# Kernel tuning notes

Hardware: AMD Instinct MI355X
Metric: run time of the kernel (lower is better)

The kernel has to match this reference:

```python
import jax, jax.numpy as jnp
import numpy as np

B, S, P, N, V = 8, 16, 32, 2048, 2562
K_SAMPLE = 500      # samples_per_slot
K_NEAREST = 3
MIN_DIST = 0.5
FALLOFF = 5.0
GW, SW, RW = 0.7, 0.3, 0.2


def _icosphere(level=4):
    t = (1.0 + 5.0 ** 0.5) / 2.0
    v = np.array([[-1, t, 0], [1, t, 0], [-1, -t, 0], [1, -t, 0],
                  [0, -1, t], [0, 1, t], [0, -1, -t], [0, 1, -t],
                  [t, 0, -1], [t, 0, 1], [-t, 0, -1], [-t, 0, 1]], dtype=np.float64)
    v /= np.linalg.norm(v, axis=1, keepdims=True)
    f = [[0, 11, 5], [0, 5, 1], [0, 1, 7], [0, 7, 10], [0, 10, 11],
         [1, 5, 9], [5, 11, 4], [11, 10, 2], [10, 7, 6], [7, 1, 8],
         [3, 9, 4], [3, 4, 2], [3, 2, 6], [3, 6, 8], [3, 8, 9],
         [4, 9, 5], [2, 4, 11], [6, 2, 10], [8, 6, 7], [9, 8, 1]]
    verts = [x for x in v]
    for _ in range(level):
        cache = {}
        def mid(a, b):
            key = (min(a, b), max(a, b))
            if key in cache:
                return cache[key]
            m = verts[a] + verts[b]
            m = m / np.linalg.norm(m)
            verts.append(m)
            cache[key] = len(verts) - 1
            return cache[key]
        nf = []
        for a, b, c in f:
            ab, bc, ca = mid(a, b), mid(b, c), mid(c, a)
            nf += [[a, ab, ca], [b, bc, ab], [c, ca, bc], [ab, bc, ca]]
        f = nf
    return np.asarray(verts, dtype=np.float32)


def _euler_xyz_to_matrix(ang):
    # pytorch3d euler_angles_to_matrix(..., 'XYZ'): R = Rx(a) @ Ry(b) @ Rz(c)
    a, b, c = ang[..., 0], ang[..., 1], ang[..., 2]
    ca, sa = jnp.cos(a), jnp.sin(a)
    cb, sb = jnp.cos(b), jnp.sin(b)
    cc, sc = jnp.cos(c), jnp.sin(c)
    o, z = jnp.ones_like(a), jnp.zeros_like(a)
    sh = ang.shape[:-1] + (3, 3)
    Rx = jnp.stack([o, z, z, z, ca, -sa, z, sa, ca], -1).reshape(sh)
    Ry = jnp.stack([cb, z, sb, z, o, z, -sb, z, cb], -1).reshape(sh)
    Rz = jnp.stack([cc, -sc, z, sc, cc, z, z, z, o], -1).reshape(sh)
    return Rx @ Ry @ Rz


def _cdist2(x, y):
    # squared euclidean distances: x [..., n, 3], y [..., m, 3] -> [..., n, m]
    x2 = (x * x).sum(-1)[..., :, None]
    y2 = (y * y).sum(-1)[..., None, :]
    return jnp.maximum(x2 + y2 - 2.0 * jnp.einsum('...nd,...md->...nm', x, y), 0.0)


def _forward(scales, transforms, prototype_weights, prototype_offsets, target_pcl, verts):
    # --- transform_mesh ---
    R = _euler_xyz_to_matrix(transforms[..., 3:])          # [B,S,P,3,3]
    deformed = verts[None] + prototype_offsets              # [P,V,3]
    rotated = jnp.einsum('pvj,bspij->bspvi', deformed, R)   # verts @ R^T
    scaled = rotated * scales[:, :, None, None, :]          # [B,S,P,V,3]
    translated = scaled + transforms[:, :, :, None, :3]
    final = jnp.einsum('bspvi,bsp->bsvi', translated, prototype_weights)  # [B,S,V,3]

    # --- hybrid chamfer loss ---
    pred = final[:, :, :K_SAMPLE, :]                        # deterministic per-slot samples
    pred_flat = pred.reshape(B, S * K_SAMPLE, 3)
    # global: target -> all predicted points, mean of K nearest squared dists
    d2g = _cdist2(target_pcl, pred_flat)                    # [B,N,S*K]
    knn = -jax.lax.top_k(-d2g, K_NEAREST)[0]
    global_loss = knn.mean()
    # per-slot: each slot's points -> target, nearest neighbor squared dist
    d2s = _cdist2(pred, target_pcl[:, None])                # [B,S,K,N]
    per_slot_loss = d2s.min(-1).mean()
    # centroid repulsion
    cent = final.mean(axis=2)                               # [B,S,3]
    eye = jnp.eye(S, dtype=final.dtype)
    d = jnp.sqrt(_cdist2(cent, cent) + eye)                 # eye keeps diag grads finite
    rep = jnp.exp(FALLOFF * jnp.maximum(MIN_DIST - d, 0.0)) * (1.0 - eye)
    rep_loss = (rep.sum(axis=(1, 2)) / (S * (S - 1))).mean()

    return GW * global_loss + SW * per_slot_loss + RW * rep_loss


def setup_inputs() -> dict:
    key = jax.random.key(0)
    ks = jax.random.split(key, 5)
    scales = jax.random.uniform(ks[0], (B, S, 1), jnp.float32) * 0.5 + 0.5
    transforms = jax.random.normal(ks[1], (B, S, P, 6), jnp.float32)
    w = jax.random.uniform(ks[2], (B, S, P), jnp.float32) + 1e-3
    prototype_weights = w / w.sum(-1, keepdims=True)
    prototype_offsets = jax.random.normal(ks[3], (P, V, 3), jnp.float32) * 0.1
    target_pcl = jax.random.normal(ks[4], (B, N, 3), jnp.float32)
    verts = jnp.asarray(_icosphere(4))                      # [2562,3]
    return {"scales": scales, "transforms": transforms,
            "prototype_weights": prototype_weights,
            "prototype_offsets": prototype_offsets,
            "target_pcl": target_pcl, "verts": verts}


def reference(scales, transforms, prototype_weights, prototype_offsets, target_pcl, verts):
    return _forward(scales, transforms, prototype_weights, prototype_offsets, target_pcl, verts)
```

## Files before the change

kernel.cpp:

```cpp
#include <hip/hip_runtime.h>
#include <math.h>

namespace {
constexpr int cB = 8, cS = 16, cP = 32, cN = 2048, cV = 2562;
constexpr int cK = 500;
constexpr int cJ = cS * cK;
constexpr int cJP = 8192;
constexpr float FINF = 3.402823466e+38f;

constexpr int OFF_TF   = 0;
constexpr int OFF_PF   = 131072;
constexpr int OFF_PSP  = 655360;
constexpr int OFF_T3   = 2752512;
constexpr int OFF_VBAR = 4849664;
constexpr int OFF_OBAR = 4849668;
constexpr int OFF_SM   = 4849792;
constexpr int OFF_SC   = 4886656;
constexpr int OFF_GM   = 4887040;
constexpr int OFF_PS   = 4887104;
}

typedef __attribute__((ext_vector_type(8))) short bf16x8;
typedef __attribute__((ext_vector_type(4))) float f32x4;

__device__ __forceinline__ float block_sum(float v, float* red, int tid) {
  red[tid] = v;
  __syncthreads();
  for (int s = 128; s > 0; s >>= 1) {
    if (tid < s) red[tid] += red[tid + s];
    __syncthreads();
  }
  return red[0];
}

__device__ __forceinline__ void top3_insert(float& t0, float& t1, float& t2, float d) {
  const float n1 = __builtin_amdgcn_fmed3f(t0, t1, d);
  const float n2 = __builtin_amdgcn_fmed3f(t1, t2, d);
  t0 = fminf(t0, d);
  t1 = n1;
  t2 = n2;
}

__device__ __forceinline__ unsigned short f2bf(float x) {
  unsigned b = __float_as_uint(x);
  return (unsigned short)((b + 0x7FFFu + ((b >> 16) & 1u)) >> 16);
}
__device__ __forceinline__ float bf2f(unsigned short u) {
  return __uint_as_float(((unsigned)u) << 16);
}

__global__ void __launch_bounds__(256) k_front(const float* __restrict__ scales,
                                               const float* __restrict__ transforms,
                                               const float* __restrict__ pw,
                                               const float* __restrict__ offs,
                                               const float* __restrict__ verts,
                                               const float* __restrict__ target,
                                               float* __restrict__ ws) {
  const int blk = blockIdx.x;
  const int tid = threadIdx.x;
  const unsigned short ONE = 0x3F80;
  if (blk <= cP) {
    __shared__ float red[256];
    const float* src = (blk < cP) ? (offs + blk * cV * 3) : verts;
    float acc0 = 0.f, acc1 = 0.f, acc2 = 0.f;
    for (int v = tid; v < cV; v += 256) {
      acc0 += src[v * 3 + 0];
      acc1 += src[v * 3 + 1];
      acc2 += src[v * 3 + 2];
    }
    float* dst = (blk < cP) ? (ws + OFF_OBAR + blk * 3) : (ws + OFF_VBAR);
    float a[3] = {acc0, acc1, acc2};
    for (int c = 0; c < 3; ++c) {
      float s = block_sum(a[c], red, tid);
      if (tid == 0) dst[c] = s / (float)cV;
      __syncthreads();
    }
  } else if (blk <= cP + 64) {
    const int idx = (blk - (cP + 1)) * 256 + tid;
    const float x = target[idx * 3 + 0];
    const float y = target[idx * 3 + 1];
    const float z = target[idx * 3 + 2];
    const unsigned short thx = f2bf(x), thy = f2bf(y), thz = f2bf(z);
    const unsigned short tlx = f2bf(x - bf2f(thx));
    const unsigned short tly = f2bf(y - bf2f(thy));
    const unsigned short tlz = f2bf(z - bf2f(thz));
    const float ht = 0.5f * fmaf(x, x, fmaf(y, y, z * z));
    const unsigned short hth = f2bf(ht);
    const unsigned short htl = f2bf(ht - bf2f(hth));
    unsigned short f[16] = {thx, thy, thz, thx, thy, thz, tlx, tly, tlz,
                            ONE, ONE, hth, htl, 0, 0, 0};
    float4* dst = (float4*)(ws + OFF_TF) + idx * 2;
    dst[0] = *(const float4*)&f[0];
    dst[1] = *(const float4*)&f[8];
  } else if (blk <= cP + 64 + cB * cS) {
    const int bs = blk - (cP + 65);
    const int b = bs >> 4, s = bs & 15;
    __shared__ float sM[cP][9];
    __shared__ float sC[3];
    __shared__ float sWT[cP][3];
    if (tid < cP) {
      const int p = tid;
      const float* t = transforms + (bs * cP + p) * 6;
      const float w = pw[bs * cP + p];
      const float sc = scales[bs];
      const float a = t[3], bb = t[4], c = t[5];
      const float ca = cosf(a), sa = sinf(a);
      const float cb = cosf(bb), sb = sinf(bb);
      const float cg = cosf(c), sg = sinf(c);
      const float f = w * sc;
      sM[p][0] = f * (cb * cg);
      sM[p][1] = f * (-cb * sg);
      sM[p][2] = f * (sb);
      sM[p][3] = f * (ca * sg + sa * sb * cg);
      sM[p][4] = f * (ca * cg - sa * sb * sg);
      sM[p][5] = f * (-sa * cb);
      sM[p][6] = f * (sa * sg - ca * sb * cg);
      sM[p][7] = f * (sa * cg + ca * sb * sg);
      sM[p][8] = f * (ca * cb);
      sWT[p][0] = w * t[0];
      sWT[p][1] = w * t[1];
      sWT[p][2] = w * t[2];
    }
    __syncthreads();
    if (tid < 3) {
      float s2 = 0.f;
      for (int p = 0; p < cP; ++p) s2 += sWT[p][tid];
      sC[tid] = s2;
    }
    __syncthreads();
    if (tid < cP * 9) ws[OFF_SM + bs * 288 + tid] = ((const float*)sM)[tid];
    if (tid < 3) ws[OFF_SC + bs * 3 + tid] = sC[tid];
    for (int k = tid; k < cK; k += 256) {
      const float x0 = verts[k * 3 + 0], x1 = verts[k * 3 + 1], x2 = verts[k * 3 + 2];
      float a0 = sC[0], a1 = sC[1], a2 = sC[2];
#pragma unroll 8
      for (int p = 0; p < cP; ++p) {
        const float* o = offs + (p * cV + k) * 3;
        const float d0 = x0 + o[0], d1 = x1 + o[1], d2 = x2 + o[2];
        a0 = fmaf(sM[p][0], d0, fmaf(sM[p][1], d1, fmaf(sM[p][2], d2, a0)));
        a1 = fmaf(sM[p][3], d0, fmaf(sM[p][4], d1, fmaf(sM[p][5], d2, a1)));
        a2 = fmaf(sM[p][6], d0, fmaf(sM[p][7], d1, fmaf(sM[p][8], d2, a2)));
      }
      const unsigned short phx = f2bf(a0), phy = f2bf(a1), phz = f2bf(a2);
      const unsigned short plx = f2bf(a0 - bf2f(phx));
      const unsigned short ply = f2bf(a1 - bf2f(phy));
      const unsigned short plz = f2bf(a2 - bf2f(phz));
      const float hp = 0.5f * fmaf(a0, a0, fmaf(a1, a1, a2 * a2));
      const unsigned short hph = f2bf(hp);
      const unsigned short hpl = f2bf(hp - bf2f(hph));
      unsigned short f[16] = {
          (unsigned short)(phx ^ 0x8000), (unsigned short)(phy ^ 0x8000),
          (unsigned short)(phz ^ 0x8000), (unsigned short)(plx ^ 0x8000),
          (unsigned short)(ply ^ 0x8000), (unsigned short)(plz ^ 0x8000),
          (unsigned short)(phx ^ 0x8000), (unsigned short)(phy ^ 0x8000),
          (unsigned short)(phz ^ 0x8000), hph, hpl, ONE, ONE, 0, 0, 0};
      float4* dst = (float4*)(ws + OFF_PF) + (b * cJP + s * cK + k) * 2;
      dst[0] = *(const float4*)&f[0];
      dst[1] = *(const float4*)&f[8];
    }
  } else {
    for (int i = tid; i < cB * (cJP - cJ); i += 256) {
      const int b = i / (cJP - cJ);
      const int j = cJ + i % (cJP - cJ);
      unsigned short f[16] = {0};
      f[9] = f2bf(30000.0f);
      float4* dst = (float4*)(ws + OFF_PF) + (b * cJP + j) * 2;
      dst[0] = *(const float4*)&f[0];
      dst[1] = *(const float4*)&f[8];
    }
  }
}

__global__ void __launch_bounds__(256) k_distm(float* __restrict__ ws) {
  __shared__ unsigned short sFrag[1024 * 16 + 16];
  __shared__ float sMin[4][514];
  const int blk = blockIdx.x;
  const int tid = threadIdx.x;
  const int e = blk & 7;
  const int tg = (blk >> 3) & 15;
  const int b = blk >> 7;
  {
    const float4* src = (const float4*)(ws + OFF_PF) + (b * cJP + e * 1024) * 2;
    float4* dst = (float4*)sFrag;
    for (int i = tid; i < 2048; i += 256) dst[i] = src[i];
    if (tid < 16) sFrag[1024 * 16 + tid] = 0;
  }
  const int w = tid >> 6, lane = tid & 63;
  const int lcol = lane & 15, lh = lane >> 4;
  for (int i = lane; i < 512; i += 64) sMin[w][i] = FINF;
  __syncthreads();

  const int half = w >> 1;
  const int tgBase = tg * 128 + (w & 1) * 64;
  const f32x4 zf = {0.f, 0.f, 0.f, 0.f};
  bf16x8 afr0, afr1, afr2, afr3;
  {
    const float4* tf = (const float4*)(ws + OFF_TF);
    float4 z4 = make_float4(0.f, 0.f, 0.f, 0.f);
    float4 v0 = z4, v1 = z4, v2 = z4, v3 = z4;
    if (lh < 2) {
      const int base = (b * cN + tgBase + lcol) * 2 + lh;
      v0 = tf[base + 0 * 32];
      v1 = tf[base + 1 * 32];
      v2 = tf[base + 2 * 32];
      v3 = tf[base + 3 * 32];
    }
    afr0 = __builtin_bit_cast(bf16x8, v0);
    afr1 = __builtin_bit_cast(bf16x8, v1);
    afr2 = __builtin_bit_cast(bf16x8, v2);
    afr3 = __builtin_bit_cast(bf16x8, v3);
  }
  float T0[4][4], T1[4][4], T2[4][4];
#pragma unroll
  for (int m = 0; m < 4; ++m)
#pragma unroll
    for (int r = 0; r < 4; ++r) { T0[m][r] = FINF; T1[m][r] = FINF; T2[m][r] = FINF; }

  int bidx = (lh < 2) ? ((half * 512 + lcol) * 16 + lh * 8) : (1024 * 16);
  const int bstep = (lh < 2) ? 256 : 0;

#pragma unroll 2
  for (int t = 0; t < 32; ++t) {
    const bf16x8 bfr = *(const bf16x8*)(&sFrag[bidx]);
    bidx += bstep;
    f32x4 c0 = __builtin_amdgcn_mfma_f32_16x16x32_bf16(afr0, bfr, zf, 0, 0, 0);
    f32x4 c1 = __builtin_amdgcn_mfma_f32_16x16x32_bf16(afr1, bfr, zf, 0, 0, 0);
    f32x4 c2 = __builtin_amdgcn_mfma_f32_16x16x32_bf16(afr2, bfr, zf, 0, 0, 0);
    f32x4 c3 = __builtin_amdgcn_mfma_f32_16x16x32_bf16(afr3, bfr, zf, 0, 0, 0);
#pragma unroll
    for (int r = 0; r < 4; ++r) top3_insert(T0[0][r], T1[0][r], T2[0][r], c0[r]);
#pragma unroll
    for (int r = 0; r < 4; ++r) top3_insert(T0[1][r], T1[1][r], T2[1][r], c1[r]);
#pragma unroll
    for (int r = 0; r < 4; ++r) top3_insert(T0[2][r], T1[2][r], T2[2][r], c2[r]);
#pragma unroll
    for (int r = 0; r < 4; ++r) top3_insert(T0[3][r], T1[3][r], T2[3][r], c3[r]);
    float v = fminf(fminf(fminf(c0[0], c0[1]), fminf(c0[2], c0[3])),
                    fminf(fminf(c1[0], c1[1]), fminf(c1[2], c1[3])));
    v = fminf(v, fminf(fminf(fminf(c2[0], c2[1]), fminf(c2[2], c2[3])),
                       fminf(fminf(c3[0], c3[1]), fminf(c3[2], c3[3]))));
    v = fminf(v, __shfl_xor(v, 16));
    v = fminf(v, __shfl_xor(v, 32));
    const int si = t * 16 + lcol;
    sMin[w][si] = fminf(sMin[w][si], v);
  }
  {
    const int slot = tg * 2 + (w & 1);
    float* dst = ws + OFF_PSP + (b * 32 + slot) * cJP + e * 1024 + half * 512;
    for (int i = lane; i < 512; i += 64) dst[i] = sMin[w][i];
  }
  for (int mask = 1; mask < 16; mask <<= 1) {
#pragma unroll
    for (int m = 0; m < 4; ++m)
#pragma unroll
      for (int r = 0; r < 4; ++r) {
        const float y0 = __shfl_xor(T0[m][r], mask);
        const float y1 = __shfl_xor(T1[m][r], mask);
        const float y2 = __shfl_xor(T2[m][r], mask);
        top3_insert(T0[m][r], T1[m][r], T2[m][r], y0);
        top3_insert(T0[m][r], T1[m][r], T2[m][r], y1);
        top3_insert(T0[m][r], T1[m][r], T2[m][r], y2);
      }
  }
  if (lcol == 0) {
    const int slice = e * 2 + half;
#pragma unroll
    for (int m = 0; m < 4; ++m)
#pragma unroll
      for (int r = 0; r < 4; ++r) {
        const int tgt = tgBase + m * 16 + lh * 4 + r;
        float* dst = ws + OFF_T3 + ((b * 16 + slice) * cN + tgt) * 4;
        dst[0] = T0[m][r];
        dst[1] = T1[m][r];
        dst[2] = T2[m][r];
      }
  }
}

__global__ void __launch_bounds__(256) k_merge(float* __restrict__ ws) {
  __shared__ float red[256];
  const int blk = blockIdx.x;
  const int tid = threadIdx.x;
  if (blk < 64) {
    const int idx = blk * 256 + tid;
    const int b = idx >> 11, n = idx & 2047;
    float t0 = FINF, t1 = FINF, t2 = FINF;
#pragma unroll
    for (int e = 0; e < 16; ++e) {
      const float* src = ws + OFF_T3 + ((b * 16 + e) * cN + n) * 4;
      top3_insert(t0, t1, t2, src[0]);
      top3_insert(t0, t1, t2, src[1]);
      top3_insert(t0, t1, t2, src[2]);
    }
    const float d0 = fmaxf(2.f * t0, 0.f);
    const float d1 = fmaxf(2.f * t1, 0.f);
    const float d2 = fmaxf(2.f * t2, 0.f);
    const float s = block_sum(d0 + d1 + d2, red, tid);
    if (tid == 0) ws[OFF_GM + blk] = s;
  } else {
    const int rb = blk - 64;
    const int b = rb >> 5;
    const int jb = rb & 31;
    const int j = jb * 256 + tid;
    float contrib = 0.f;
    if (j < cJ) {
      float m = FINF;
#pragma unroll
      for (int s = 0; s < 32; ++s)
        m = fminf(m, ws[OFF_PSP + (b * 32 + s) * cJP + j]);
      contrib = fmaxf(2.f * m, 0.f);
    }
    const float s = block_sum(contrib, red, tid);
    if (tid == 0) ws[OFF_PS + b * 32 + jb] = s;
  }
}

__global__ void __launch_bounds__(256) k_final(float* __restrict__ ws, float* __restrict__ out) {
  __shared__ float red[256];
  __shared__ float scent[cB * cS * 3];
  const int tid = threadIdx.x;
  if (tid < cB * cS) {
    const int bs = tid;
    const float* M = ws + OFF_SM + bs * 288;
    const float* vb = ws + OFF_VBAR;
    float c0 = ws[OFF_SC + bs * 3 + 0];
    float c1 = ws[OFF_SC + bs * 3 + 1];
    float c2 = ws[OFF_SC + bs * 3 + 2];
#pragma unroll 8
    for (int p = 0; p < cP; ++p) {
      const float* ob = ws + OFF_OBAR + p * 3;
      const float d0 = vb[0] + ob[0], d1 = vb[1] + ob[1], d2 = vb[2] + ob[2];
      c0 = fmaf(M[p * 9 + 0], d0, fmaf(M[p * 9 + 1], d1, fmaf(M[p * 9 + 2], d2, c0)));
      c1 = fmaf(M[p * 9 + 3], d0, fmaf(M[p * 9 + 4], d1, fmaf(M[p * 9 + 5], d2, c1)));
      c2 = fmaf(M[p * 9 + 6], d0, fmaf(M[p * 9 + 7], d1, fmaf(M[p * 9 + 8], d2, c2)));
    }
    scent[bs * 3 + 0] = c0;
    scent[bs * 3 + 1] = c1;
    scent[bs * 3 + 2] = c2;
  }
  __syncthreads();
  float acc = 0.f;
  for (int idx = tid; idx < cB * cS * cS; idx += 256) {
    const int b = idx / (cS * cS);
    const int r = idx % (cS * cS);
    const int i = r / cS, jj = r % cS;
    if (i == jj) continue;
    const float* ci = scent + (b * cS + i) * 3;
    const float* cj = scent + (b * cS + jj) * 3;
    const float dx = ci[0] - cj[0], dy = ci[1] - cj[1], dz = ci[2] - cj[2];
    const float d = sqrtf(fmaf(dx, dx, fmaf(dy, dy, dz * dz)));
    acc += expf(5.0f * fmaxf(0.5f - d, 0.0f));
  }
  const float repsum = block_sum(acc, red, tid);
  __syncthreads();
  const float gsum = block_sum((tid < 64) ? ws[OFF_GM + tid] : 0.f, red, tid);
  __syncthreads();
  const float pssum = block_sum(ws[OFF_PS + tid], red, tid);
  if (tid == 0) {
    const float global_loss = gsum / (float)(cB * cN * 3);
    const float per_slot = pssum / (float)(cB * cS * cK);
    const float rep = repsum / (float)(cB * cS * (cS - 1));
    out[0] = 0.7f * global_loss + 0.3f * per_slot + 0.2f * rep;
  }
}

extern "C" void kernel_launch(void* const* d_in, const int* in_sizes, int n_in,
                              void* d_out, int out_size, void* d_ws, size_t ws_size,
                              hipStream_t stream) {
  const float* scales     = (const float*)d_in[0];
  const float* transforms = (const float*)d_in[1];
  const float* pw         = (const float*)d_in[2];
  const float* offs       = (const float*)d_in[3];
  const float* target     = (const float*)d_in[4];
  const float* verts      = (const float*)d_in[5];
  float* out = (float*)d_out;
  float* ws = (float*)d_ws;

  k_front<<<cP + 1 + 64 + cB * cS + 1, 256, 0, stream>>>(scales, transforms, pw, offs,
                                                         verts, target, ws);
  k_distm<<<1024, 256, 0, stream>>>(ws);
  k_merge<<<64 + 256, 256, 0, stream>>>(ws);
  k_final<<<1, 256, 0, stream>>>(ws, out);
}
```

Measured before the change: 69.25 us.

## Split distance blocks into smaller 128-thread tiles with merge-network top-3 reduction

Restructures the distance kernel so each block takes 512 sample columns with 2 waves instead of 1024 columns with 4 waves, launching twice as many blocks. Each wave now covers all its columns directly, which removes the zero-padded lanes and the per-iteration read-modify-write of the shared-memory column minimum. The cross-lane top-3 reduction becomes a sorted-merge min/max network instead of three sequential inserts. The top-3 workspace moves to a structure-of-arrays layout so the merge kernel reads coalesced. The cost is more blocks and a larger partial-top3 buffer to merge, 48 values per target instead of 48 strided loads.

```diff
diff --git a/kernel.cpp b/kernel.cpp
--- a/kernel.cpp
+++ b/kernel.cpp
@@ -6,18 +6,19 @@
 constexpr int cK = 500;
 constexpr int cJ = cS * cK;
 constexpr int cJP = 8192;
+constexpr int cBN = cB * cN;
 constexpr float FINF = 3.402823466e+38f;
 
 constexpr int OFF_TF   = 0;
 constexpr int OFF_PF   = 131072;
 constexpr int OFF_PSP  = 655360;
 constexpr int OFF_T3   = 2752512;
-constexpr int OFF_VBAR = 4849664;
-constexpr int OFF_OBAR = 4849668;
-constexpr int OFF_SM   = 4849792;
-constexpr int OFF_SC   = 4886656;
-constexpr int OFF_GM   = 4887040;
-constexpr int OFF_PS   = 4887104;
+constexpr int OFF_VBAR = 3538944;
+constexpr int OFF_OBAR = 3538948;
+constexpr int OFF_SM   = 3539072;
+constexpr int OFF_SC   = 3575936;
+constexpr int OFF_GM   = 3576320;
+constexpr int OFF_PS   = 3576384;
 }
 
 typedef __attribute__((ext_vector_type(8))) short bf16x8;
@@ -171,27 +172,23 @@
   }
 }
 
-__global__ void __launch_bounds__(256) k_distm(float* __restrict__ ws) {
-  __shared__ unsigned short sFrag[1024 * 16 + 16];
-  __shared__ float sMin[4][514];
+__global__ void __launch_bounds__(128, 4) k_distm(float* __restrict__ ws) {
+  __shared__ unsigned short sFrag[512 * 16];
+  __shared__ float sMin[2][512];
   const int blk = blockIdx.x;
   const int tid = threadIdx.x;
-  const int e = blk & 7;
-  const int tg = (blk >> 3) & 15;
-  const int b = blk >> 7;
+  const int e = blk & 15;
+  const int tg = (blk >> 4) & 15;
+  const int b = blk >> 8;
   {
-    const float4* src = (const float4*)(ws + OFF_PF) + (b * cJP + e * 1024) * 2;
+    const float4* src = (const float4*)(ws + OFF_PF) + (b * cJP + e * 512) * 2;
     float4* dst = (float4*)sFrag;
-    for (int i = tid; i < 2048; i += 256) dst[i] = src[i];
-    if (tid < 16) sFrag[1024 * 16 + tid] = 0;
-  }
+    for (int i = tid; i < 1024; i += 128) dst[i] = src[i];
+  }
+  __syncthreads();
   const int w = tid >> 6, lane = tid & 63;
   const int lcol = lane & 15, lh = lane >> 4;
-  for (int i = lane; i < 512; i += 64) sMin[w][i] = FINF;
-  __syncthreads();
-
-  const int half = w >> 1;
-  const int tgBase = tg * 128 + (w & 1) * 64;
+  const int tgBase = tg * 128 + w * 64;
   const f32x4 zf = {0.f, 0.f, 0.f, 0.f};
   bf16x8 afr0, afr1, afr2, afr3;
   {
@@ -210,69 +207,64 @@
     afr2 = __builtin_bit_cast(bf16x8, v2);
     afr3 = __builtin_bit_cast(bf16x8, v3);
   }
-  float T0[4][4], T1[4][4], T2[4][4];
-#pragma unroll
-  for (int m = 0; m < 4; ++m)
-#pragma unroll
-    for (int r = 0; r < 4; ++r) { T0[m][r] = FINF; T1[m][r] = FINF; T2[m][r] = FINF; }
-
-  int bidx = (lh < 2) ? ((half * 512 + lcol) * 16 + lh * 8) : (1024 * 16);
-  const int bstep = (lh < 2) ? 256 : 0;
-
-#pragma unroll 2
+  float T0[16], T1[16], T2[16];
+#pragma unroll
+  for (int q = 0; q < 16; ++q) { T0[q] = FINF; T1[q] = FINF; T2[q] = FINF; }
+
+  const int bbase = lcol * 16 + (lh & 1) * 8;
+#pragma unroll 8
   for (int t = 0; t < 32; ++t) {
-    const bf16x8 bfr = *(const bf16x8*)(&sFrag[bidx]);
-    bidx += bstep;
+    const bf16x8 bfr = *(const bf16x8*)(&sFrag[t * 256 + bbase]);
     f32x4 c0 = __builtin_amdgcn_mfma_f32_16x16x32_bf16(afr0, bfr, zf, 0, 0, 0);
     f32x4 c1 = __builtin_amdgcn_mfma_f32_16x16x32_bf16(afr1, bfr, zf, 0, 0, 0);
     f32x4 c2 = __builtin_amdgcn_mfma_f32_16x16x32_bf16(afr2, bfr, zf, 0, 0, 0);
     f32x4 c3 = __builtin_amdgcn_mfma_f32_16x16x32_bf16(afr3, bfr, zf, 0, 0, 0);
 #pragma unroll
-    for (int r = 0; r < 4; ++r) top3_insert(T0[0][r], T1[0][r], T2[0][r], c0[r]);
-#pragma unroll
-    for (int r = 0; r < 4; ++r) top3_insert(T0[1][r], T1[1][r], T2[1][r], c1[r]);
-#pragma unroll
-    for (int r = 0; r < 4; ++r) top3_insert(T0[2][r], T1[2][r], T2[2][r], c2[r]);
-#pragma unroll
-    for (int r = 0; r < 4; ++r) top3_insert(T0[3][r], T1[3][r], T2[3][r], c3[r]);
-    float v = fminf(fminf(fminf(c0[0], c0[1]), fminf(c0[2], c0[3])),
-                    fminf(fminf(c1[0], c1[1]), fminf(c1[2], c1[3])));
-    v = fminf(v, fminf(fminf(fminf(c2[0], c2[1]), fminf(c2[2], c2[3])),
-                       fminf(fminf(c3[0], c3[1]), fminf(c3[2], c3[3]))));
+    for (int r = 0; r < 4; ++r) top3_insert(T0[0 + r], T1[0 + r], T2[0 + r], c0[r]);
+#pragma unroll
+    for (int r = 0; r < 4; ++r) top3_insert(T0[4 + r], T1[4 + r], T2[4 + r], c1[r]);
+#pragma unroll
+    for (int r = 0; r < 4; ++r) top3_insert(T0[8 + r], T1[8 + r], T2[8 + r], c2[r]);
+#pragma unroll
+    for (int r = 0; r < 4; ++r) top3_insert(T0[12 + r], T1[12 + r], T2[12 + r], c3[r]);
+    const float v0 = fminf(fminf(c0[0], c0[1]), c0[2]);
+    const float v1 = fminf(fminf(c0[3], c1[0]), c1[1]);
+    const float v2 = fminf(fminf(c1[2], c1[3]), c2[0]);
+    const float v3 = fminf(fminf(c2[1], c2[2]), c2[3]);
+    const float v4 = fminf(fminf(c3[0], c3[1]), c3[2]);
+    float v = fminf(fminf(fminf(v0, v1), fminf(v2, v3)), fminf(v4, c3[3]));
     v = fminf(v, __shfl_xor(v, 16));
     v = fminf(v, __shfl_xor(v, 32));
-    const int si = t * 16 + lcol;
-    sMin[w][si] = fminf(sMin[w][si], v);
+    sMin[w][t * 16 + lcol] = v;
   }
   {
-    const int slot = tg * 2 + (w & 1);
-    float* dst = ws + OFF_PSP + (b * 32 + slot) * cJP + e * 1024 + half * 512;
+    float* dst = ws + OFF_PSP + (b * 32 + tg * 2 + w) * cJP + e * 512;
     for (int i = lane; i < 512; i += 64) dst[i] = sMin[w][i];
   }
+#pragma unroll
   for (int mask = 1; mask < 16; mask <<= 1) {
 #pragma unroll
+    for (int q = 0; q < 16; ++q) {
+      const float b0 = __shfl_xor(T0[q], mask);
+      const float b1 = __shfl_xor(T1[q], mask);
+      const float b2 = __shfl_xor(T2[q], mask);
+      const float a0 = T0[q], a1 = T1[q], a2 = T2[q];
+      T0[q] = fminf(a0, b0);
+      T1[q] = fminf(fminf(a1, b1), fmaxf(a0, b0));
+      T2[q] = fminf(fminf(a2, b2), fminf(fmaxf(a0, b1), fmaxf(a1, b0)));
+    }
+  }
+  if (lcol == 0) {
+    const int slice = e;
+#pragma unroll
     for (int m = 0; m < 4; ++m)
 #pragma unroll
       for (int r = 0; r < 4; ++r) {
-        const float y0 = __shfl_xor(T0[m][r], mask);
-        const float y1 = __shfl_xor(T1[m][r], mask);
-        const float y2 = __shfl_xor(T2[m][r], mask);
-        top3_insert(T0[m][r], T1[m][r], T2[m][r], y0);
-        top3_insert(T0[m][r], T1[m][r], T2[m][r], y1);
-        top3_insert(T0[m][r], T1[m][r], T2[m][r], y2);
-      }
-  }
-  if (lcol == 0) {
-    const int slice = e * 2 + half;
-#pragma unroll
-    for (int m = 0; m < 4; ++m)
-#pragma unroll
-      for (int r = 0; r < 4; ++r) {
-        const int tgt = tgBase + m * 16 + lh * 4 + r;
-        float* dst = ws + OFF_T3 + ((b * 16 + slice) * cN + tgt) * 4;
-        dst[0] = T0[m][r];
-        dst[1] = T1[m][r];
-        dst[2] = T2[m][r];
+        const int q = m * 4 + r;
+        const int idx = b * cN + tgBase + m * 16 + lh * 4 + r;
+        ws[OFF_T3 + (slice * 3 + 0) * cBN + idx] = T0[q];
+        ws[OFF_T3 + (slice * 3 + 1) * cBN + idx] = T1[q];
+        ws[OFF_T3 + (slice * 3 + 2) * cBN + idx] = T2[q];
       }
   }
 }
@@ -283,15 +275,11 @@
   const int tid = threadIdx.x;
   if (blk < 64) {
     const int idx = blk * 256 + tid;
-    const int b = idx >> 11, n = idx & 2047;
+    const float* plane = ws + OFF_T3;
     float t0 = FINF, t1 = FINF, t2 = FINF;
-#pragma unroll
-    for (int e = 0; e < 16; ++e) {
-      const float* src = ws + OFF_T3 + ((b * 16 + e) * cN + n) * 4;
-      top3_insert(t0, t1, t2, src[0]);
-      top3_insert(t0, t1, t2, src[1]);
-      top3_insert(t0, t1, t2, src[2]);
-    }
+#pragma unroll 8
+    for (int q = 0; q < 48; ++q)
+      top3_insert(t0, t1, t2, plane[q * cBN + idx]);
     const float d0 = fmaxf(2.f * t0, 0.f);
     const float d1 = fmaxf(2.f * t1, 0.f);
     const float d2 = fmaxf(2.f * t2, 0.f);
@@ -378,7 +366,7 @@
 
   k_front<<<cP + 1 + 64 + cB * cS + 1, 256, 0, stream>>>(scales, transforms, pw, offs,
                                                          verts, target, ws);
-  k_distm<<<1024, 256, 0, stream>>>(ws);
+  k_distm<<<2048, 128, 0, stream>>>(ws);
   k_merge<<<64 + 256, 256, 0, stream>>>(ws);
   k_final<<<1, 256, 0, stream>>>(ws, out);
 }
```

After: 66.53 us. 3.9% less time.
